# Kernel optimization log

Hardware: AMD Instinct MI355X
Metric: run time of the kernel (lower is better)

The kernel has to match this reference:

```python
import jax, jax.numpy as jnp
import numpy as np

B, T, NB = 8192, 18, 6
EH, DH = 256, 256
NIN = NB + 1  # encoder GRU input: bits + feedback scalar


def gru_cell(x, h, Wih, Whh, bih, bhh):
    # PyTorch GRU cell: gates ordered (r, z, n)
    gi = x @ Wih.T + bih
    gh = h @ Whh.T + bhh
    ir, iz, inn = jnp.split(gi, 3, axis=-1)
    hr, hz, hn = jnp.split(gh, 3, axis=-1)
    r = jax.nn.sigmoid(ir + hr)
    z = jax.nn.sigmoid(iz + hz)
    n = jnp.tanh(inn + r * hn)
    return (1.0 - z) * n + z * h


def run_gru_dir(seq, Wih, Whh, bih, bhh, reverse):
    # seq: [T, B, D] -> hidden outputs [T, B, H] (aligned to original time order)
    Bn, H = seq.shape[1], Whh.shape[1]
    def step(h, x):
        h2 = gru_cell(x, h, Wih, Whh, bih, bhh)
        return h2, h2
    _, outs = jax.lax.scan(step, jnp.zeros((Bn, H), seq.dtype), seq, reverse=reverse)
    return outs


def setup_inputs() -> dict:
    key = jax.random.key(0)
    ks = jax.random.split(key, 40)
    def w(k, shape, fan):
        s = 1.0 / np.sqrt(fan)
        return jax.random.uniform(k, shape, jnp.float32, -s, s)
    inp = {}
    inp['b'] = (jax.random.uniform(ks[0], (B, NB)) < 0.5).astype(jnp.float32)
    inp['noise1'] = jax.random.normal(ks[1], (B, T, 1), jnp.float32)
    inp['noise2'] = jax.random.normal(ks[2], (B, T, 1), jnp.float32)
    # encoder GRU (2 layers, unidirectional)
    inp['enc_Wih0'] = w(ks[3], (3 * EH, NIN), EH); inp['enc_Whh0'] = w(ks[4], (3 * EH, EH), EH)
    inp['enc_bih0'] = w(ks[5], (3 * EH,), EH);     inp['enc_bhh0'] = w(ks[6], (3 * EH,), EH)
    inp['enc_Wih1'] = w(ks[7], (3 * EH, EH), EH);  inp['enc_Whh1'] = w(ks[8], (3 * EH, EH), EH)
    inp['enc_bih1'] = w(ks[9], (3 * EH,), EH);     inp['enc_bhh1'] = w(ks[10], (3 * EH,), EH)
    inp['enc_lin_W'] = w(ks[11], (1, EH), EH);     inp['enc_lin_b'] = w(ks[12], (1,), EH)
    inp['weight_power'] = jnp.ones((T,), jnp.float32)
    # decoder GRU (2 layers, bidirectional)
    inp['dec_Wih0f'] = w(ks[13], (3 * DH, 1), DH);      inp['dec_Whh0f'] = w(ks[14], (3 * DH, DH), DH)
    inp['dec_bih0f'] = w(ks[15], (3 * DH,), DH);        inp['dec_bhh0f'] = w(ks[16], (3 * DH,), DH)
    inp['dec_Wih0b'] = w(ks[17], (3 * DH, 1), DH);      inp['dec_Whh0b'] = w(ks[18], (3 * DH, DH), DH)
    inp['dec_bih0b'] = w(ks[19], (3 * DH,), DH);        inp['dec_bhh0b'] = w(ks[20], (3 * DH,), DH)
    inp['dec_Wih1f'] = w(ks[21], (3 * DH, 2 * DH), DH); inp['dec_Whh1f'] = w(ks[22], (3 * DH, DH), DH)
    inp['dec_bih1f'] = w(ks[23], (3 * DH,), DH);        inp['dec_bhh1f'] = w(ks[24], (3 * DH,), DH)
    inp['dec_Wih1b'] = w(ks[25], (3 * DH, 2 * DH), DH); inp['dec_Whh1b'] = w(ks[26], (3 * DH, DH), DH)
    inp['dec_bih1b'] = w(ks[27], (3 * DH,), DH);        inp['dec_bhh1b'] = w(ks[28], (3 * DH,), DH)
    inp['dec_lin_W'] = w(ks[29], (NB, 2 * DH), 2 * DH); inp['dec_lin_b'] = w(ks[30], (NB,), 2 * DH)
    inp['weight_merge'] = jnp.ones((T, 2), jnp.float32)
    return inp


def reference(b, noise1, noise2,
              enc_Wih0, enc_Whh0, enc_bih0, enc_bhh0,
              enc_Wih1, enc_Whh1, enc_bih1, enc_bhh1,
              enc_lin_W, enc_lin_b, weight_power,
              dec_Wih0f, dec_Whh0f, dec_bih0f, dec_bhh0f,
              dec_Wih0b, dec_Whh0b, dec_bih0b, dec_bhh0b,
              dec_Wih1f, dec_Whh1f, dec_bih1f, dec_bhh1f,
              dec_Wih1b, dec_Whh1b, dec_bih1b, dec_bhh1b,
              dec_lin_W, dec_lin_b, weight_merge):
    Bn = b.shape[0]
    Tn = weight_power.shape[0]
    # power-normalized per-step weights: sqrt(w^2 * T / sum(w^2))
    wp = jnp.sqrt(weight_power ** 2 * Tn / jnp.sum(weight_power ** 2))

    def enc_step(carry, xs):
        h0, h1, z = carry
        n1, n2, wpt = xs
        inp = jnp.concatenate([b, z], axis=1)            # [B, NB+1]
        h0n = gru_cell(inp, h0, enc_Wih0, enc_Whh0, enc_bih0, enc_bhh0)
        h1n = gru_cell(h0n, h1, enc_Wih1, enc_Whh1, enc_bih1, enc_bhh1)
        xt = jnp.tanh(h1n @ enc_lin_W.T + enc_lin_b)     # [B, 1]
        xn = (xt - jnp.mean(xt)) / jnp.std(xt, ddof=1)   # training-mode batch norm over whole tensor
        y = xn * wpt + n1                                # received symbol
        return (h0n, h1n, y + n2), y                     # feedback z = y + noise2

    carry0 = (jnp.zeros((Bn, EH), b.dtype), jnp.zeros((Bn, EH), b.dtype), jnp.zeros((Bn, 1), b.dtype))
    xs = (jnp.swapaxes(noise1, 0, 1), jnp.swapaxes(noise2, 0, 1), wp)
    _, y_seq = jax.lax.scan(enc_step, carry0, xs)        # [T, B, 1]

    # bidirectional 2-layer decoder GRU over y
    o0f = run_gru_dir(y_seq, dec_Wih0f, dec_Whh0f, dec_bih0f, dec_bhh0f, False)
    o0b = run_gru_dir(y_seq, dec_Wih0b, dec_Whh0b, dec_bih0b, dec_bhh0b, True)
    s1 = jnp.concatenate([o0f, o0b], axis=-1)            # [T, B, 2*DH]
    o1f = run_gru_dir(s1, dec_Wih1f, dec_Whh1f, dec_bih1f, dec_bhh1f, False)
    o1b = run_gru_dir(s1, dec_Wih1b, dec_Whh1b, dec_bih1b, dec_bhh1b, True)

    # attention_type == 5: learned weighted merge over time, per direction
    wf = jnp.sqrt(weight_merge[:, 0] ** 2 * Tn / jnp.sum(weight_merge[:, 0] ** 2))
    wb = jnp.sqrt(weight_merge[:, 1] ** 2 * Tn / jnp.sum(weight_merge[:, 1] ** 2))
    rf = jnp.einsum('tbh,t->bh', o1f, wf)
    rb = jnp.einsum('tbh,t->bh', o1b, wb)
    rc = jnp.concatenate([rf, rb], axis=1)               # [B, 2*DH]
    out = jax.nn.sigmoid(rc @ dec_lin_W.T + dec_lin_b)   # bit_vector output -> sigmoid
    return out.reshape(Bn, -1, 1)
```

## Files before the change

kernel.cpp:

```cpp
#include <hip/hip_runtime.h>
#include <hip/hip_bf16.h>
#include <math.h>

#define BN_ 8192
#define TT 18
#define NBITS 6
#define HH 256
#define G3 768

typedef __hip_bfloat16 hbf16;
typedef __bf16 bf16x8 __attribute__((ext_vector_type(8)));
typedef float f32x4 __attribute__((ext_vector_type(4)));

__device__ inline float sigm(float x){ return 1.0f/(1.0f + expf(-x)); }
__device__ inline float ldx(const void* p, int i, int bf){
    if(bf){ unsigned short u = ((const unsigned short*)p)[i]; return __uint_as_float(((unsigned)u)<<16); }
    return ((const float*)p)[i];
}
__device__ inline __bf16 f2b(float f){ hbf16 h = __float2bfloat16(f); return *reinterpret_cast<__bf16*>(&h); }
__device__ inline float b2f(__bf16 b){ unsigned short u = *reinterpret_cast<unsigned short*>(&b); return __uint_as_float(((unsigned)u)<<16); }
__device__ inline unsigned pack2(float a, float b){
    hbf16 lo = __float2bfloat16(a), hi = __float2bfloat16(b);
    return (unsigned)*(unsigned short*)&lo | ((unsigned)*(unsigned short*)&hi << 16);
}

__global__ __launch_bounds__(256) void fillz(float* __restrict__ p, int n){
    for(int i = blockIdx.x*256 + threadIdx.x; i < n; i += gridDim.x*256) p[i] = 0.0f;
}
__global__ __launch_bounds__(256) void fillb(__bf16* __restrict__ p, int n){
    for(int i = blockIdx.x*256 + threadIdx.x; i < n; i += gridDim.x*256) p[i] = f2b(0.0f);
}

__global__ void prep_w(const void* wp, const void* wm, unsigned* flag,
                       float* wpn, float* wfn, float* wbn){
    if(threadIdx.x==0 && blockIdx.x==0){
        unsigned w0 = *(const unsigned*)wp;
        int bf = ((w0 >> 16) == (w0 & 0xFFFFu)) ? 1 : 0;
        flag[0] = (unsigned)bf;
        float s=0; for(int t=0;t<TT;t++){ float v=ldx(wp,t,bf); s += v*v; }
        for(int t=0;t<TT;t++){ float v=ldx(wp,t,bf); wpn[t] = sqrtf(v*v*TT/s); }
        float sf=0, sb=0;
        for(int t=0;t<TT;t++){ float f=ldx(wm,2*t,bf), b=ldx(wm,2*t+1,bf); sf += f*f; sb += b*b; }
        for(int t=0;t<TT;t++){
            float f=ldx(wm,2*t,bf), b=ldx(wm,2*t+1,bf);
            wfn[t] = sqrtf(f*f*TT/sf);
            wbn[t] = sqrtf(b*b*TT/sb);
        }
    }
}

struct CJ { const void* src; void* dst; int n; int K; int mode; };
struct CJs { CJ j[20]; };
__global__ __launch_bounds__(256) void conv_all(CJs J, const unsigned* __restrict__ flagp){
    const int bf = (int)*flagp;
    CJ c = J.j[blockIdx.y];
    for(int i = blockIdx.x*256 + threadIdx.x; i < c.n; i += gridDim.x*256){
        if(c.mode==1){
            int row = i / c.K, k = i - row*c.K;
            int g = row>>8, jj = row&255;
            int prow = ((jj>>4)*48) + g*16 + (jj&15);
            ((__bf16*)c.dst)[(size_t)prow*c.K + k] = f2b(ldx(c.src, i, bf));
        }else if(c.mode==2){
            int t = i >> 13, b = i & (BN_-1);
            ((float*)c.dst)[i] = ldx(c.src, b*TT + t, bf);
        }else{
            ((float*)c.dst)[i] = ldx(c.src, i, bf);
        }
    }
}

struct FQ {
    const __bf16* A1; const __bf16* W1; int K1;
    const __bf16* A2; const __bf16* W2; int K2;
    const float* bgi; const float* bgh;
    const __bf16* h; __bf16* hout;
    const void* bits; const void* wih0raw; const void* bih0raw; const float* zf;
    const void* linw; float* xt;
    const float* y; const void* wihraw; const void* bihraw; __bf16* s1t;
};
struct FQ2 { FQ q[2]; };

template<int MODE>
__global__ __launch_bounds__(256,3) void fused_step(FQ2 PP, const unsigned* __restrict__ flagp){
    const FQ P = PP.q[blockIdx.z];
    const int bf = (int)*flagp;
    __shared__ __align__(16) char smem[28672];
    __bf16* As = (__bf16*)smem;
    __bf16* Ws = (__bf16*)(smem + 16384);
    float*  T  = (float*)smem;
    const int tid = threadIdx.x;
    const int mt = blockIdx.x*8 + (blockIdx.y>>3);
    const int jt = blockIdx.y & 7;
    const int m0 = mt*128;
    const int n0 = jt*96;
    const int lane = tid&63, wv = tid>>6;
    const int wrow = wv>>1, wcol = wv&1;
    const int q = lane>>4, n15 = lane&15;

    f32x4 accR[4], accZ[4], accN1[4], accN2[4];
    #pragma unroll
    for(int i=0;i<4;i++){ accR[i]=(f32x4){0,0,0,0}; accZ[i]=(f32x4){0,0,0,0};
                          accN1[i]=(f32x4){0,0,0,0}; accN2[i]=(f32x4){0,0,0,0}; }

    #pragma unroll
    for(int ph = 0; ph < 2; ph++){
        if(ph==0 && MODE!=1) continue;
        const __bf16* __restrict__ A = ph ? P.A2 : P.A1;
        const __bf16* __restrict__ W = ph ? P.W2 : P.W1;
        const int K = ph ? P.K2 : P.K1;
        for(int k0=0;k0<K;k0+=64){
            #pragma unroll
            for(int s=0;s<4;s++){
                int c = tid + 256*s;
                int row = c>>3, qc = c&7, col = qc ^ ((row>>1)&7);
                *(uint4*)&As[row*64 + col*8] = *(const uint4*)(A + (size_t)(m0+row)*K + k0 + qc*8);
            }
            #pragma unroll
            for(int s=0;s<3;s++){
                int c = tid + 256*s;
                int row = c>>3, qc = c&7, col = qc ^ ((row>>1)&7);
                *(uint4*)&Ws[row*64 + col*8] = *(const uint4*)(W + (size_t)(n0+row)*K + k0 + qc*8);
            }
            __syncthreads();
            #pragma unroll
            for(int ks=0;ks<2;ks++){
                const int cq = ks*4 + q;
                bf16x8 af[4], bfr[3];
                #pragma unroll
                for(int i=0;i<4;i++){
                    int R = wrow*64+i*16+n15;
                    int col = cq ^ ((R>>1)&7);
                    af[i] = *(const bf16x8*)&As[R*64 + col*8];
                }
                #pragma unroll
                for(int g=0;g<3;g++){
                    int RW = wcol*48+g*16+n15;
                    int col = cq ^ ((RW>>1)&7);
                    bfr[g] = *(const bf16x8*)&Ws[RW*64 + col*8];
                }
                #pragma unroll
                for(int i=0;i<4;i++){
                    accR[i] = __builtin_amdgcn_mfma_f32_16x16x32_bf16(af[i], bfr[0], accR[i], 0,0,0);
                    accZ[i] = __builtin_amdgcn_mfma_f32_16x16x32_bf16(af[i], bfr[1], accZ[i], 0,0,0);
                    if(ph) accN2[i] = __builtin_amdgcn_mfma_f32_16x16x32_bf16(af[i], bfr[2], accN2[i], 0,0,0);
                    else   accN1[i] = __builtin_amdgcn_mfma_f32_16x16x32_bf16(af[i], bfr[2], accN1[i], 0,0,0);
                }
            }
            __syncthreads();
        }
    }

    const int jl = wcol*16 + n15;
    const int j  = jt*32 + jl;
    const float bghr = P.bgh[j], bghz = P.bgh[256+j], bghn = P.bgh[512+j];
    float bgir=0, bgiz=0, bgin=0;
    if(MODE==1){ bgir = P.bgi[j]; bgiz = P.bgi[256+j]; bgin = P.bgi[512+j]; }
    float w0r[7], w0z[7], w0n[7];
    if(MODE==0){
        #pragma unroll
        for(int k=0;k<7;k++){
            w0r[k] = ldx(P.wih0raw, (j    )*7+k, bf);
            w0z[k] = ldx(P.wih0raw, (j+256)*7+k, bf);
            w0n[k] = ldx(P.wih0raw, (j+512)*7+k, bf);
        }
        bgir = ldx(P.bih0raw, j, bf); bgiz = ldx(P.bih0raw, j+256, bf); bgin = ldx(P.bih0raw, j+512, bf);
    }
    float wy_r=0, wy_z=0, wy_n=0;
    if(MODE==2){
        wy_r = ldx(P.wihraw, j, bf); wy_z = ldx(P.wihraw, j+256, bf); wy_n = ldx(P.wihraw, j+512, bf);
        bgir = ldx(P.bihraw, j, bf); bgiz = ldx(P.bihraw, j+256, bf); bgin = ldx(P.bihraw, j+512, bf);
    }
    const float linwj = (MODE==1) ? ldx(P.linw, j, bf) : 0.0f;

    #pragma unroll
    for(int i=0;i<4;i++){
        const int rbl = wrow*64 + i*16 + q*4;
        float vred[4];
        #pragma unroll
        for(int r=0;r<4;r++){
            const int row_l = rbl + r;
            const int row = m0 + row_l;
            float gir, giz, gin;
            if(MODE==1){
                gir = bgir; giz = bgiz; gin = accN1[i][r] + bgin;
            }else if(MODE==0){
                gir = bgir; giz = bgiz; gin = bgin;
                #pragma unroll
                for(int k=0;k<NBITS;k++){
                    float bv = ldx(P.bits, row*NBITS+k, bf);
                    gir += bv*w0r[k]; giz += bv*w0z[k]; gin += bv*w0n[k];
                }
                float zb = P.zf[row];
                gir += zb*w0r[6]; giz += zb*w0z[6]; gin += zb*w0n[6];
            }else{
                float yv = P.y[row];
                gir = yv*wy_r + bgir; giz = yv*wy_z + bgiz; gin = yv*wy_n + bgin;
            }
            float rr = sigm(gir + accR[i][r] + bghr);
            float zz = sigm(giz + accZ[i][r] + bghz);
            float nn = tanhf(gin + rr*(accN2[i][r] + bghn));
            float hold = b2f(P.h[(size_t)row*HH + j]);
            float hn = (1.0f - zz)*nn + zz*hold;
            T[row_l*33 + jl] = hn;
            if(MODE==1) vred[r] = hn*linwj;
        }
        if(MODE==1){
            #pragma unroll
            for(int r=0;r<4;r++){
                float v = vred[r];
                #pragma unroll
                for(int m=1;m<16;m<<=1) v += __shfl_xor(v, m);
                if(n15==0) atomicAdd(&P.xt[m0+rbl+r], v);
            }
        }
    }
    __syncthreads();

    const int rw2 = tid>>2, cw = tid&3;
    #pragma unroll
    for(int pass=0; pass<2; pass++){
        const int row_l = pass*64 + rw2;
        const int row = m0 + row_l;
        float v[8];
        #pragma unroll
        for(int u=0;u<8;u++) v[u] = T[row_l*33 + cw*8 + u];
        uint4 pkv = { pack2(v[0],v[1]), pack2(v[2],v[3]), pack2(v[4],v[5]), pack2(v[6],v[7]) };
        *(uint4*)&P.hout[(size_t)row*HH + jt*32 + cw*8] = pkv;
        if(MODE==2) *(uint4*)&P.s1t[(size_t)row*512 + jt*32 + cw*8] = pkv;
    }
}

struct MJ {
    int mode; int K;
    const __bf16* A; const __bf16* W; const float* bias;
    __bf16* gout;
    const __bf16* gin;
    const __bf16* h; __bf16* hout; float* racc; const float* wct;
};
struct MJ4 { MJ j[4]; };

__global__ __launch_bounds__(256,3) void fused_mix(MJ4 PP){
    const MJ J = PP.j[blockIdx.z];
    __shared__ __align__(16) char smem[28672];
    __bf16* As = (__bf16*)smem;
    __bf16* Ws = (__bf16*)(smem + 16384);
    float*  T  = (float*)smem;
    const int tid = threadIdx.x;
    const int mt = blockIdx.x*8 + (blockIdx.y>>3);
    const int jt = blockIdx.y & 7;
    const int m0 = mt*128, n0 = jt*96;
    const int lane = tid&63, wv = tid>>6;
    const int wrow = wv>>1, wcol = wv&1;
    const int q = lane>>4, n15 = lane&15;

    f32x4 acc[3][4];
    #pragma unroll
    for(int g=0;g<3;g++)
        #pragma unroll
        for(int i=0;i<4;i++) acc[g][i]=(f32x4){0,0,0,0};

    const __bf16* __restrict__ A = J.A;
    const __bf16* __restrict__ W = J.W;
    const int K = J.K;
    for(int k0=0;k0<K;k0+=64){
        #pragma unroll
        for(int s=0;s<4;s++){
            int c = tid + 256*s;
            int row = c>>3, qc = c&7, col = qc ^ ((row>>1)&7);
            *(uint4*)&As[row*64 + col*8] = *(const uint4*)(A + (size_t)(m0+row)*K + k0 + qc*8);
        }
        #pragma unroll
        for(int s=0;s<3;s++){
            int c = tid + 256*s;
            int row = c>>3, qc = c&7, col = qc ^ ((row>>1)&7);
            *(uint4*)&Ws[row*64 + col*8] = *(const uint4*)(W + (size_t)(n0+row)*K + k0 + qc*8);
        }
        __syncthreads();
        #pragma unroll
        for(int ks=0;ks<2;ks++){
            const int cq = ks*4 + q;
            bf16x8 af[4], bfr[3];
            #pragma unroll
            for(int i=0;i<4;i++){
                int R = wrow*64+i*16+n15;
                int col = cq ^ ((R>>1)&7);
                af[i] = *(const bf16x8*)&As[R*64 + col*8];
            }
            #pragma unroll
            for(int g=0;g<3;g++){
                int RW = wcol*48+g*16+n15;
                int col = cq ^ ((RW>>1)&7);
                bfr[g] = *(const bf16x8*)&Ws[RW*64 + col*8];
            }
            #pragma unroll
            for(int i=0;i<4;i++){
                acc[0][i] = __builtin_amdgcn_mfma_f32_16x16x32_bf16(af[i], bfr[0], acc[0][i], 0,0,0);
                acc[1][i] = __builtin_amdgcn_mfma_f32_16x16x32_bf16(af[i], bfr[1], acc[1][i], 0,0,0);
                acc[2][i] = __builtin_amdgcn_mfma_f32_16x16x32_bf16(af[i], bfr[2], acc[2][i], 0,0,0);
            }
        }
        __syncthreads();
    }

    const int jl = wcol*16 + n15;
    const int j  = jt*32 + jl;
    const float bg0 = J.bias[j], bg1 = J.bias[256+j], bg2 = J.bias[512+j];
    const int rw2 = tid>>2, cw = tid&3;

    if(J.mode==4){
        const float bgs[3] = {bg0, bg1, bg2};
        for(int g=0; g<3; g++){
            if(g) __syncthreads();
            #pragma unroll
            for(int i=0;i<4;i++){
                const int rbl = wrow*64 + i*16 + q*4;
                #pragma unroll
                for(int r=0;r<4;r++) T[(rbl+r)*33 + jl] = acc[g][i][r] + bgs[g];
            }
            __syncthreads();
            #pragma unroll
            for(int pass=0; pass<2; pass++){
                const int row_l = pass*64 + rw2;
                const int row = m0 + row_l;
                float v[8];
                #pragma unroll
                for(int u=0;u<8;u++) v[u] = T[row_l*33 + cw*8 + u];
                uint4 pkv = { pack2(v[0],v[1]), pack2(v[2],v[3]), pack2(v[4],v[5]), pack2(v[6],v[7]) };
                *(uint4*)&J.gout[(size_t)row*G3 + jt*96 + g*32 + cw*8] = pkv;
            }
        }
    }else{
        #pragma unroll
        for(int i=0;i<4;i++){
            const int rbl = wrow*64 + i*16 + q*4;
            #pragma unroll
            for(int r=0;r<4;r++){
                const int row_l = rbl + r;
                const int row = m0 + row_l;
                const __bf16* gb = J.gin + (size_t)row*G3 + jt*96;
                float gir = b2f(gb[jl]), giz = b2f(gb[32+jl]), gnn = b2f(gb[64+jl]);
                float rr = sigm(gir + acc[0][i][r] + bg0);
                float zz = sigm(giz + acc[1][i][r] + bg1);
                float nn = tanhf(gnn + rr*(acc[2][i][r] + bg2));
                float hold = b2f(J.h[(size_t)row*HH + j]);
                float hn = (1.0f - zz)*nn + zz*hold;
                T[row_l*33 + jl] = hn;
            }
        }
        __syncthreads();
        const float wct = J.wct[0];
        #pragma unroll
        for(int pass=0; pass<2; pass++){
            const int row_l = pass*64 + rw2;
            const int row = m0 + row_l;
            float v[8];
            #pragma unroll
            for(int u=0;u<8;u++) v[u] = T[row_l*33 + cw*8 + u];
            uint4 pkv = { pack2(v[0],v[1]), pack2(v[2],v[3]), pack2(v[4],v[5]), pack2(v[6],v[7]) };
            *(uint4*)&J.hout[(size_t)row*HH + jt*32 + cw*8] = pkv;
            float* rp = &J.racc[(size_t)row*HH + jt*32 + cw*8];
            float4 a0 = *(float4*)rp, a1 = *(float4*)(rp+4);
            a0.x += wct*v[0]; a0.y += wct*v[1]; a0.z += wct*v[2]; a0.w += wct*v[3];
            a1.x += wct*v[4]; a1.y += wct*v[5]; a1.z += wct*v[6]; a1.w += wct*v[7];
            *(float4*)rp = a0; *(float4*)(rp+4) = a1;
        }
    }
}

__global__ __launch_bounds__(1024) void stats_emit(float* __restrict__ xt, const void* __restrict__ lb,
        const float* __restrict__ wpn, int t, const float* __restrict__ n1t, const float* __restrict__ n2t,
        float* __restrict__ yseq, float* __restrict__ zf, const unsigned* __restrict__ flagp){
    const int bf = (int)*flagp;
    const float lbv = ldx(lb, 0, bf);
    int tid = threadIdx.x;
    float s=0.0f, ss=0.0f;
    for(int i=tid;i<BN_;i+=1024){ float v = tanhf(xt[i] + lbv); s += v; ss += v*v; }
    #pragma unroll
    for(int o=32;o;o>>=1){ s += __shfl_down(s,o); ss += __shfl_down(ss,o); }
    __shared__ float S[16], SS[16], stm[2];
    if((tid&63)==0){ S[tid>>6]=s; SS[tid>>6]=ss; }
    __syncthreads();
    if(tid==0){
        float a=0.0f, b=0.0f;
        for(int i=0;i<16;i++){ a+=S[i]; b+=SS[i]; }
        float mean = a/(float)BN_;
        float var = (b - (float)BN_*mean*mean)/(float)(BN_-1);
        stm[0]=mean; stm[1]=1.0f/sqrtf(var);
    }
    __syncthreads();
    const float mean=stm[0], rs=stm[1], wt=wpn[t];
    for(int i=tid;i<BN_;i+=1024){
        float v = tanhf(xt[i] + lbv);
        float y = (v-mean)*rs*wt + n1t[i];
        yseq[(size_t)t*BN_ + i] = y;
        zf[i] = y + n2t[i];
        xt[i] = 0.0f;
    }
}

__global__ __launch_bounds__(256) void final_k(const float* __restrict__ rf, const float* __restrict__ rb,
        const void* __restrict__ W, const void* __restrict__ bias, void* __restrict__ out,
        const unsigned* __restrict__ flagp){
    const int bf = (int)*flagp;
    int lane = threadIdx.x & 63;
    int row = blockIdx.x*4 + (threadIdx.x>>6);
    float a[6] = {};
    #pragma unroll
    for(int i=0;i<4;i++){
        int c = lane + 64*i;
        float xf = rf[(size_t)row*HH + c];
        float xb = rb[(size_t)row*HH + c];
        #pragma unroll
        for(int k=0;k<6;k++) a[k] += xf*ldx(W, k*512 + c, bf) + xb*ldx(W, k*512 + 256 + c, bf);
    }
    #pragma unroll
    for(int o=32;o;o>>=1){
        #pragma unroll
        for(int k=0;k<6;k++) a[k] += __shfl_down(a[k], o);
    }
    if(lane==0){
        #pragma unroll
        for(int k=0;k<6;k++){
            float v = sigm(a[k] + ldx(bias,k,bf));
            if(bf) ((hbf16*)out)[(size_t)row*6+k] = __float2bfloat16(v);
            else   ((float*)out)[(size_t)row*6+k] = v;
        }
    }
}

extern "C" void kernel_launch(void* const* d_in, const int* in_sizes, int n_in,
                              void* d_out, int out_size, void* d_ws, size_t ws_size,
                              hipStream_t stream)
{
    (void)in_sizes; (void)n_in; (void)out_size;
    const void* bits  = d_in[0];
    const void* n1    = d_in[1];
    const void* n2    = d_in[2];
    const void* eWih0 = d_in[3];
    const void* eWhh0 = d_in[4];
    const void* ebih0 = d_in[5];
    const void* ebhh0 = d_in[6];
    const void* eWih1 = d_in[7];
    const void* eWhh1 = d_in[8];
    const void* ebih1 = d_in[9];
    const void* ebhh1 = d_in[10];
    const void* elinW = d_in[11];
    const void* elinb = d_in[12];
    const void* wpow  = d_in[13];
    const void* dWih0f= d_in[14];
    const void* dWhh0f= d_in[15];
    const void* dbih0f= d_in[16];
    const void* dbhh0f= d_in[17];
    const void* dWih0b= d_in[18];
    const void* dWhh0b= d_in[19];
    const void* dbih0b= d_in[20];
    const void* dbhh0b= d_in[21];
    const void* dWih1f= d_in[22];
    const void* dWhh1f= d_in[23];
    const void* dbih1f= d_in[24];
    const void* dbhh1f= d_in[25];
    const void* dWih1b= d_in[26];
    const void* dWhh1b= d_in[27];
    const void* dbih1b= d_in[28];
    const void* dbhh1b= d_in[29];
    const void* dlinW = d_in[30];
    const void* dlinb = d_in[31];
    const void* wmrg  = d_in[32];

    float* base = (float*)d_ws;
    size_t off = 0;
    auto alloc  = [&](size_t n){ float* p = base + off; off += (n + 63) & ~(size_t)63; return p; };
    auto allocb = [&](size_t n){ __bf16* p = (__bf16*)(base + off); off += ((n/2) + 63) & ~(size_t)63; return p; };
    unsigned* flag = (unsigned*)alloc(64);
    float* wpn = alloc(TT); float* wfn = alloc(TT); float* wbn = alloc(TT);
    const int WK = HH*G3;
    __bf16* WeHH0 = allocb(WK);  __bf16* WeIH1 = allocb(WK);  __bf16* WeHH1 = allocb(WK);
    __bf16* Wd0f  = allocb(WK);  __bf16* Wd0b  = allocb(WK);
    __bf16* Wd1fI = allocb(2*WK);__bf16* Wd1bI = allocb(2*WK);
    __bf16* Wd1fH = allocb(WK);  __bf16* Wd1bH = allocb(WK);
    float* BeHH0 = alloc(G3); float* BeIH1 = alloc(G3); float* BeHH1 = alloc(G3);
    float* Bd0f  = alloc(G3); float* Bd0b  = alloc(G3);
    float* Bd1fI = alloc(G3); float* Bd1bI = alloc(G3);
    float* Bd1fH = alloc(G3); float* Bd1bH = alloc(G3);
    const size_t NH = (size_t)BN_*HH;
    __bf16* X0 = allocb(NH);  __bf16* X1 = allocb(NH);
    __bf16* Y0 = allocb(NH);  __bf16* Y1 = allocb(NH);
    float* rf  = alloc(NH);
    float* rb  = alloc(NH);
    float* xt  = alloc(BN_);
    float* zf  = alloc(BN_);
    float* yseq= alloc((size_t)TT*BN_);
    float* n1t = alloc((size_t)TT*BN_);
    float* n2t = alloc((size_t)TT*BN_);
    __bf16* giF0 = allocb((size_t)BN_*G3);  __bf16* giF1 = allocb((size_t)BN_*G3);
    __bf16* giB0 = allocb((size_t)BN_*G3);  __bf16* giB1 = allocb((size_t)BN_*G3);
    __bf16* s1 = allocb((size_t)TT*BN_*512);
    size_t need = off*sizeof(float);
    if(ws_size < need) return;

    prep_w<<<1,64,0,stream>>>(wpow, wmrg, flag, wpn, wfn, wbn);
    CJs J;
    const void* ws_src[20] = {eWhh0,eWih1,eWhh1,dWhh0f,dWhh0b,dWih1f,dWih1b,dWhh1f,dWhh1b,
                              ebhh0,ebih1,ebhh1,dbhh0f,dbhh0b,dbih1f,dbih1b,dbhh1f,dbhh1b, n1, n2};
    void* ws_dst[20] = {WeHH0,WeIH1,WeHH1,Wd0f,Wd0b,Wd1fI,Wd1bI,Wd1fH,Wd1bH,
                        BeHH0,BeIH1,BeHH1,Bd0f,Bd0b,Bd1fI,Bd1bI,Bd1fH,Bd1bH, n1t, n2t};
    int ws_n[20] = {WK,WK,WK,WK,WK,2*WK,2*WK,WK,WK, G3,G3,G3,G3,G3,G3,G3,G3,G3, TT*BN_, TT*BN_};
    int ws_K[20] = {256,256,256,256,256,512,512,256,256, 0,0,0,0,0,0,0,0,0, 0,0};
    int ws_m[20] = {1,1,1,1,1,1,1,1,1, 0,0,0,0,0,0,0,0,0, 2,2};
    for(int i=0;i<20;i++){ J.j[i] = {ws_src[i], ws_dst[i], ws_n[i], ws_K[i], ws_m[i]}; }
    conv_all<<<dim3(768,20),256,0,stream>>>(J, flag);
    fillb<<<1024,256,0,stream>>>(X0, (int)NH);
    fillb<<<1024,256,0,stream>>>(Y0, (int)NH);
    fillz<<<32,256,0,stream>>>(xt, BN_);
    fillz<<<32,256,0,stream>>>(zf, BN_);

    dim3 g1(8, 64, 1), g2(8, 64, 2), g4(8, 64, 4);
    __bf16* X[2] = {X0, X1};
    __bf16* Y[2] = {Y0, Y1};
    __bf16* giF[2] = {giF0, giF1};
    __bf16* giB[2] = {giB0, giB1};

    int p = 0;
    for(int t=0;t<TT;t++){
        FQ2 P0{}; FQ2 P1{};
        FQ& a = P0.q[0];
        a.A2=X[p]; a.W2=WeHH0; a.K2=HH; a.bgh=BeHH0; a.h=X[p]; a.hout=X[1-p];
        a.bits=bits; a.wih0raw=eWih0; a.bih0raw=ebih0; a.zf=zf;
        fused_step<0><<<g1,256,0,stream>>>(P0, flag);
        FQ& b = P1.q[0];
        b.A1=X[1-p]; b.W1=WeIH1; b.K1=HH; b.A2=Y[p]; b.W2=WeHH1; b.K2=HH;
        b.bgi=BeIH1; b.bgh=BeHH1; b.h=Y[p]; b.hout=Y[1-p];
        b.linw=elinW; b.xt=xt;
        fused_step<1><<<g1,256,0,stream>>>(P1, flag);
        stats_emit<<<1,1024,0,stream>>>(xt, elinb, wpn, t, n1t+(size_t)t*BN_, n2t+(size_t)t*BN_,
                                        yseq, zf, flag);
        p ^= 1;
    }

    fillb<<<1024,256,0,stream>>>(X0, (int)NH);
    fillb<<<1024,256,0,stream>>>(Y0, (int)NH);
    p = 0;
    for(int i=0;i<TT;i++){
        int tf = i, tb = TT-1-i;
        FQ2 P{};
        FQ& a = P.q[0];
        a.A2=X[p]; a.W2=Wd0f; a.K2=HH; a.bgh=Bd0f; a.h=X[p]; a.hout=X[1-p];
        a.y=yseq+(size_t)tf*BN_; a.wihraw=dWih0f; a.bihraw=dbih0f; a.s1t=s1+(size_t)tf*BN_*512;
        FQ& b = P.q[1];
        b.A2=Y[p]; b.W2=Wd0b; b.K2=HH; b.bgh=Bd0b; b.h=Y[p]; b.hout=Y[1-p];
        b.y=yseq+(size_t)tb*BN_; b.wihraw=dWih0b; b.bihraw=dbih0b; b.s1t=s1+(size_t)tb*BN_*512+256;
        fused_step<2><<<g2,256,0,stream>>>(P, flag);
        p ^= 1;
    }

    fillb<<<1024,256,0,stream>>>(X0, (int)NH);
    fillb<<<1024,256,0,stream>>>(Y0, (int)NH);
    fillz<<<1024,256,0,stream>>>(rf, (int)(2*NH));
    {
        MJ4 P{};
        P.j[0] = {4, 512, s1, Wd1fI, Bd1fI, giF[0], nullptr, nullptr, nullptr, nullptr, nullptr};
        P.j[1] = {4, 512, s1+(size_t)(TT-1)*BN_*512, Wd1bI, Bd1bI, giB[0], nullptr, nullptr, nullptr, nullptr, nullptr};
        fused_mix<<<g2,256,0,stream>>>(P);
    }
    p = 0;
    for(int i=0;i<TT;i++){
        int tf = i, tb = TT-1-i;
        MJ4 P{};
        P.j[0] = {5, 256, X[p], Wd1fH, Bd1fH, nullptr, giF[i&1], X[p], X[1-p], rf, wfn+tf};
        P.j[1] = {5, 256, Y[p], Wd1bH, Bd1bH, nullptr, giB[i&1], Y[p], Y[1-p], rb, wbn+tb};
        if(i < TT-1){
            P.j[2] = {4, 512, s1+(size_t)(tf+1)*BN_*512, Wd1fI, Bd1fI, giF[(i+1)&1],
                      nullptr, nullptr, nullptr, nullptr, nullptr};
            P.j[3] = {4, 512, s1+(size_t)(tb-1)*BN_*512, Wd1bI, Bd1bI, giB[(i+1)&1],
                      nullptr, nullptr, nullptr, nullptr, nullptr};
            fused_mix<<<g4,256,0,stream>>>(P);
        }else{
            fused_mix<<<g2,256,0,stream>>>(P);
        }
        p ^= 1;
    }

    final_k<<<BN_/4,256,0,stream>>>(rf, rb, dlinW, dlinb, d_out, flag);
}
```

Before: 1.995 ms.

## Restructure encoder and decoder layer-1 GRU step scheduling across kernels

```diff
diff --git a/kernel.cpp b/kernel.cpp
--- a/kernel.cpp
+++ b/kernel.cpp
@@ -74,9 +74,8 @@
     const __bf16* A2; const __bf16* W2; int K2;
     const float* bgi; const float* bgh;
     const __bf16* h; __bf16* hout;
-    const void* bits; const void* wih0raw; const void* bih0raw; const float* zf;
-    const void* linw; float* xt;
     const float* y; const void* wihraw; const void* bihraw; __bf16* s1t;
+    float* racc; const float* wct;
 };
 struct FQ2 { FQ q[2]; };
 
@@ -104,7 +103,7 @@
 
     #pragma unroll
     for(int ph = 0; ph < 2; ph++){
-        if(ph==0 && MODE!=1) continue;
+        if(ph==0 && MODE!=3) continue;
         const __bf16* __restrict__ A = ph ? P.A2 : P.A1;
         const __bf16* __restrict__ W = ph ? P.W2 : P.W1;
         const int K = ph ? P.K2 : P.K1;
@@ -154,44 +153,23 @@
     const int j  = jt*32 + jl;
     const float bghr = P.bgh[j], bghz = P.bgh[256+j], bghn = P.bgh[512+j];
     float bgir=0, bgiz=0, bgin=0;
-    if(MODE==1){ bgir = P.bgi[j]; bgiz = P.bgi[256+j]; bgin = P.bgi[512+j]; }
-    float w0r[7], w0z[7], w0n[7];
-    if(MODE==0){
-        #pragma unroll
-        for(int k=0;k<7;k++){
-            w0r[k] = ldx(P.wih0raw, (j    )*7+k, bf);
-            w0z[k] = ldx(P.wih0raw, (j+256)*7+k, bf);
-            w0n[k] = ldx(P.wih0raw, (j+512)*7+k, bf);
-        }
-        bgir = ldx(P.bih0raw, j, bf); bgiz = ldx(P.bih0raw, j+256, bf); bgin = ldx(P.bih0raw, j+512, bf);
-    }
+    if(MODE==3){ bgir = P.bgi[j]; bgiz = P.bgi[256+j]; bgin = P.bgi[512+j]; }
     float wy_r=0, wy_z=0, wy_n=0;
     if(MODE==2){
         wy_r = ldx(P.wihraw, j, bf); wy_z = ldx(P.wihraw, j+256, bf); wy_n = ldx(P.wihraw, j+512, bf);
         bgir = ldx(P.bihraw, j, bf); bgiz = ldx(P.bihraw, j+256, bf); bgin = ldx(P.bihraw, j+512, bf);
     }
-    const float linwj = (MODE==1) ? ldx(P.linw, j, bf) : 0.0f;
 
     #pragma unroll
     for(int i=0;i<4;i++){
         const int rbl = wrow*64 + i*16 + q*4;
-        float vred[4];
         #pragma unroll
         for(int r=0;r<4;r++){
             const int row_l = rbl + r;
             const int row = m0 + row_l;
             float gir, giz, gin;
-            if(MODE==1){
+            if(MODE==3){
                 gir = bgir; giz = bgiz; gin = accN1[i][r] + bgin;
-            }else if(MODE==0){
-                gir = bgir; giz = bgiz; gin = bgin;
-                #pragma unroll
-                for(int k=0;k<NBITS;k++){
-                    float bv = ldx(P.bits, row*NBITS+k, bf);
-                    gir += bv*w0r[k]; giz += bv*w0z[k]; gin += bv*w0n[k];
-                }
-                float zb = P.zf[row];
-                gir += zb*w0r[6]; giz += zb*w0z[6]; gin += zb*w0n[6];
             }else{
                 float yv = P.y[row];
                 gir = yv*wy_r + bgir; giz = yv*wy_z + bgiz; gin = yv*wy_n + bgin;
@@ -202,16 +180,6 @@
             float hold = b2f(P.h[(size_t)row*HH + j]);
             float hn = (1.0f - zz)*nn + zz*hold;
             T[row_l*33 + jl] = hn;
-            if(MODE==1) vred[r] = hn*linwj;
-        }
-        if(MODE==1){
-            #pragma unroll
-            for(int r=0;r<4;r++){
-                float v = vred[r];
-                #pragma unroll
-                for(int m=1;m<16;m<<=1) v += __shfl_xor(v, m);
-                if(n15==0) atomicAdd(&P.xt[m0+rbl+r], v);
-            }
         }
     }
     __syncthreads();
@@ -227,20 +195,30 @@
         uint4 pkv = { pack2(v[0],v[1]), pack2(v[2],v[3]), pack2(v[4],v[5]), pack2(v[6],v[7]) };
         *(uint4*)&P.hout[(size_t)row*HH + jt*32 + cw*8] = pkv;
         if(MODE==2) *(uint4*)&P.s1t[(size_t)row*512 + jt*32 + cw*8] = pkv;
-    }
-}
-
-struct MJ {
+        if(MODE==3){
+            const float wct = P.wct[0];
+            float* rp = &P.racc[(size_t)row*HH + jt*32 + cw*8];
+            float4 a0 = *(float4*)rp, a1 = *(float4*)(rp+4);
+            a0.x += wct*v[0]; a0.y += wct*v[1]; a0.z += wct*v[2]; a0.w += wct*v[3];
+            a1.x += wct*v[4]; a1.y += wct*v[5]; a1.z += wct*v[6]; a1.w += wct*v[7];
+            *(float4*)rp = a0; *(float4*)(rp+4) = a1;
+        }
+    }
+}
+
+struct EJ {
     int mode; int K;
     const __bf16* A; const __bf16* W; const float* bias;
+    const void* bits; const void* wih0raw; const void* bih0raw; const float* zf;
     __bf16* gout;
-    const __bf16* gin;
-    const __bf16* h; __bf16* hout; float* racc; const float* wct;
+    const __bf16* gin; const void* linw; float* xt;
+    const __bf16* h; __bf16* hout;
 };
-struct MJ4 { MJ j[4]; };
-
-__global__ __launch_bounds__(256,3) void fused_mix(MJ4 PP){
-    const MJ J = PP.j[blockIdx.z];
+struct EJ2 { EJ j[2]; };
+
+__global__ __launch_bounds__(256,3) void enc_mix(EJ2 PP, const unsigned* __restrict__ flagp){
+    const EJ J = PP.j[blockIdx.z];
+    const int bf = (int)*flagp;
     __shared__ __align__(16) char smem[28672];
     __bf16* As = (__bf16*)smem;
     __bf16* Ws = (__bf16*)(smem + 16384);
@@ -329,41 +307,79 @@
                 *(uint4*)&J.gout[(size_t)row*G3 + jt*96 + g*32 + cw*8] = pkv;
             }
         }
-    }else{
+        return;
+    }
+
+    if(J.mode==0){
+        float w0r[7], w0z[7], w0n[7];
+        #pragma unroll
+        for(int k=0;k<7;k++){
+            w0r[k] = ldx(J.wih0raw, (j    )*7+k, bf);
+            w0z[k] = ldx(J.wih0raw, (j+256)*7+k, bf);
+            w0n[k] = ldx(J.wih0raw, (j+512)*7+k, bf);
+        }
+        const float bir = ldx(J.bih0raw, j, bf), biz = ldx(J.bih0raw, j+256, bf), bin = ldx(J.bih0raw, j+512, bf);
         #pragma unroll
         for(int i=0;i<4;i++){
             const int rbl = wrow*64 + i*16 + q*4;
+            #pragma unroll
+            for(int r=0;r<4;r++){
+                const int row_l = rbl + r;
+                const int row = m0 + row_l;
+                float gir = bir, giz = biz, gin = bin;
+                #pragma unroll
+                for(int k=0;k<NBITS;k++){
+                    float bv = ldx(J.bits, row*NBITS+k, bf);
+                    gir += bv*w0r[k]; giz += bv*w0z[k]; gin += bv*w0n[k];
+                }
+                float zb = J.zf[row];
+                gir += zb*w0r[6]; giz += zb*w0z[6]; gin += zb*w0n[6];
+                float rr = sigm(gir + acc[0][i][r] + bg0);
+                float zz = sigm(giz + acc[1][i][r] + bg1);
+                float nn = tanhf(gin + rr*(acc[2][i][r] + bg2));
+                float hold = b2f(J.h[(size_t)row*HH + j]);
+                T[row_l*33 + jl] = (1.0f - zz)*nn + zz*hold;
+            }
+        }
+    }else{
+        const float linwj = ldx(J.linw, j, bf);
+        #pragma unroll
+        for(int i=0;i<4;i++){
+            const int rbl = wrow*64 + i*16 + q*4;
+            float vred[4];
             #pragma unroll
             for(int r=0;r<4;r++){
                 const int row_l = rbl + r;
                 const int row = m0 + row_l;
                 const __bf16* gb = J.gin + (size_t)row*G3 + jt*96;
-                float gir = b2f(gb[jl]), giz = b2f(gb[32+jl]), gnn = b2f(gb[64+jl]);
-                float rr = sigm(gir + acc[0][i][r] + bg0);
-                float zz = sigm(giz + acc[1][i][r] + bg1);
-                float nn = tanhf(gnn + rr*(acc[2][i][r] + bg2));
+                float ghr = b2f(gb[jl]), ghz = b2f(gb[32+jl]), ghn = b2f(gb[64+jl]);
+                float rr = sigm(acc[0][i][r] + bg0 + ghr);
+                float zz = sigm(acc[1][i][r] + bg1 + ghz);
+                float nn = tanhf(acc[2][i][r] + bg2 + rr*ghn);
                 float hold = b2f(J.h[(size_t)row*HH + j]);
                 float hn = (1.0f - zz)*nn + zz*hold;
                 T[row_l*33 + jl] = hn;
-            }
-        }
-        __syncthreads();
-        const float wct = J.wct[0];
-        #pragma unroll
-        for(int pass=0; pass<2; pass++){
-            const int row_l = pass*64 + rw2;
-            const int row = m0 + row_l;
-            float v[8];
-            #pragma unroll
-            for(int u=0;u<8;u++) v[u] = T[row_l*33 + cw*8 + u];
-            uint4 pkv = { pack2(v[0],v[1]), pack2(v[2],v[3]), pack2(v[4],v[5]), pack2(v[6],v[7]) };
-            *(uint4*)&J.hout[(size_t)row*HH + jt*32 + cw*8] = pkv;
-            float* rp = &J.racc[(size_t)row*HH + jt*32 + cw*8];
-            float4 a0 = *(float4*)rp, a1 = *(float4*)(rp+4);
-            a0.x += wct*v[0]; a0.y += wct*v[1]; a0.z += wct*v[2]; a0.w += wct*v[3];
-            a1.x += wct*v[4]; a1.y += wct*v[5]; a1.z += wct*v[6]; a1.w += wct*v[7];
-            *(float4*)rp = a0; *(float4*)(rp+4) = a1;
-        }
+                vred[r] = hn*linwj;
+            }
+            #pragma unroll
+            for(int r=0;r<4;r++){
+                float v = vred[r];
+                #pragma unroll
+                for(int m=1;m<16;m<<=1) v += __shfl_xor(v, m);
+                if(n15==0) atomicAdd(&J.xt[rbl + r + m0], v);
+            }
+        }
+    }
+    __syncthreads();
+    #pragma unroll
+    for(int pass=0; pass<2; pass++){
+        const int row_l = pass*64 + rw2;
+        const int row = m0 + row_l;
+        float v[8];
+        #pragma unroll
+        for(int u=0;u<8;u++) v[u] = T[row_l*33 + cw*8 + u];
+        uint4 pkv = { pack2(v[0],v[1]), pack2(v[2],v[3]), pack2(v[4],v[5]), pack2(v[6],v[7]) };
+        *(uint4*)&J.hout[(size_t)row*HH + jt*32 + cw*8] = pkv;
     }
 }
 
@@ -492,8 +508,7 @@
     float* yseq= alloc((size_t)TT*BN_);
     float* n1t = alloc((size_t)TT*BN_);
     float* n2t = alloc((size_t)TT*BN_);
-    __bf16* giF0 = allocb((size_t)BN_*G3);  __bf16* giF1 = allocb((size_t)BN_*G3);
-    __bf16* giB0 = allocb((size_t)BN_*G3);  __bf16* giB1 = allocb((size_t)BN_*G3);
+    __bf16* ghE = allocb((size_t)BN_*G3);
     __bf16* s1 = allocb((size_t)TT*BN_*512);
     size_t need = off*sizeof(float);
     if(ws_size < need) return;
@@ -514,24 +529,25 @@
     fillz<<<32,256,0,stream>>>(xt, BN_);
     fillz<<<32,256,0,stream>>>(zf, BN_);
 
-    dim3 g1(8, 64, 1), g2(8, 64, 2), g4(8, 64, 4);
+    dim3 g1(8, 64, 1), g2(8, 64, 2);
     __bf16* X[2] = {X0, X1};
     __bf16* Y[2] = {Y0, Y1};
-    __bf16* giF[2] = {giF0, giF1};
-    __bf16* giB[2] = {giB0, giB1};
 
     int p = 0;
     for(int t=0;t<TT;t++){
-        FQ2 P0{}; FQ2 P1{};
-        FQ& a = P0.q[0];
-        a.A2=X[p]; a.W2=WeHH0; a.K2=HH; a.bgh=BeHH0; a.h=X[p]; a.hout=X[1-p];
-        a.bits=bits; a.wih0raw=eWih0; a.bih0raw=ebih0; a.zf=zf;
-        fused_step<0><<<g1,256,0,stream>>>(P0, flag);
-        FQ& b = P1.q[0];
-        b.A1=X[1-p]; b.W1=WeIH1; b.K1=HH; b.A2=Y[p]; b.W2=WeHH1; b.K2=HH;
-        b.bgi=BeIH1; b.bgh=BeHH1; b.h=Y[p]; b.hout=Y[1-p];
-        b.linw=elinW; b.xt=xt;
-        fused_step<1><<<g1,256,0,stream>>>(P1, flag);
+        EJ2 A{};
+        EJ& a0 = A.j[0];
+        a0.mode=0; a0.K=HH; a0.A=X[p]; a0.W=WeHH0; a0.bias=BeHH0;
+        a0.bits=bits; a0.wih0raw=eWih0; a0.bih0raw=ebih0; a0.zf=zf;
+        a0.h=X[p]; a0.hout=X[1-p];
+        EJ& a1 = A.j[1];
+        a1.mode=4; a1.K=HH; a1.A=Y[p]; a1.W=WeHH1; a1.bias=BeHH1; a1.gout=ghE;
+        enc_mix<<<g2,256,0,stream>>>(A, flag);
+        EJ2 B{};
+        EJ& b0 = B.j[0];
+        b0.mode=5; b0.K=HH; b0.A=X[1-p]; b0.W=WeIH1; b0.bias=BeIH1;
+        b0.gin=ghE; b0.linw=elinW; b0.xt=xt; b0.h=Y[p]; b0.hout=Y[1-p];
+        enc_mix<<<g1,256,0,stream>>>(B, flag);
         stats_emit<<<1,1024,0,stream>>>(xt, elinb, wpn, t, n1t+(size_t)t*BN_, n2t+(size_t)t*BN_,
                                         yseq, zf, flag);
         p ^= 1;
@@ -556,27 +572,19 @@
     fillb<<<1024,256,0,stream>>>(X0, (int)NH);
     fillb<<<1024,256,0,stream>>>(Y0, (int)NH);
     fillz<<<1024,256,0,stream>>>(rf, (int)(2*NH));
-    {
-        MJ4 P{};
-        P.j[0] = {4, 512, s1, Wd1fI, Bd1fI, giF[0], nullptr, nullptr, nullptr, nullptr, nullptr};
-        P.j[1] = {4, 512, s1+(size_t)(TT-1)*BN_*512, Wd1bI, Bd1bI, giB[0], nullptr, nullptr, nullptr, nullptr, nullptr};
-        fused_mix<<<g2,256,0,stream>>>(P);
-    }
     p = 0;
     for(int i=0;i<TT;i++){
         int tf = i, tb = TT-1-i;
-        MJ4 P{};
-        P.j[0] = {5, 256, X[p], Wd1fH, Bd1fH, nullptr, giF[i&1], X[p], X[1-p], rf, wfn+tf};
-        P.j[1] = {5, 256, Y[p], Wd1bH, Bd1bH, nullptr, giB[i&1], Y[p], Y[1-p], rb, wbn+tb};
-        if(i < TT-1){
-            P.j[2] = {4, 512, s1+(size_t)(tf+1)*BN_*512, Wd1fI, Bd1fI, giF[(i+1)&1],
-                      nullptr, nullptr, nullptr, nullptr, nullptr};
-            P.j[3] = {4, 512, s1+(size_t)(tb-1)*BN_*512, Wd1bI, Bd1bI, giB[(i+1)&1],
-                      nullptr, nullptr, nullptr, nullptr, nullptr};
-            fused_mix<<<g4,256,0,stream>>>(P);
-        }else{
-            fused_mix<<<g2,256,0,stream>>>(P);
-        }
+        FQ2 P{};
+        FQ& a = P.q[0];
+        a.A1=s1+(size_t)tf*BN_*512; a.W1=Wd1fI; a.K1=512;
+        a.A2=X[p]; a.W2=Wd1fH; a.K2=HH; a.bgi=Bd1fI; a.bgh=Bd1fH; a.h=X[p]; a.hout=X[1-p];
+        a.racc=rf; a.wct=wfn+tf;
+        FQ& b = P.q[1];
+        b.A1=s1+(size_t)tb*BN_*512; b.W1=Wd1bI; b.K1=512;
+        b.A2=Y[p]; b.W2=Wd1bH; b.K2=HH; b.bgi=Bd1bI; b.bgh=Bd1bH; b.h=Y[p]; b.hout=Y[1-p];
+        b.racc=rb; b.wct=wbn+tb;
+        fused_step<3><<<g2,256,0,stream>>>(P, flag);
         p ^= 1;
     }
 
```

After: 1.993 ms. About the same (-0.1%).
